# Performance work log

Measured on AMD Instinct MI355X. Metric: run time of the kernel, lower is better.

## Reference

```python
import jax, jax.numpy as jnp
import numpy as np

B, C, H, W = 4, 256, 128, 128
HEADS, KD, VD = 8, 64, 64
EPS = 1e-5


def setup_inputs() -> dict:
    key = jax.random.key(0)
    ks = jax.random.split(key, 5)
    s = 0.02
    return {
        "x": jax.random.normal(ks[0], (B, C, H, W), dtype=jnp.float32),
        "wq": jax.random.normal(ks[1], (HEADS * KD, C), dtype=jnp.float32) * s,
        "bq": jnp.zeros((HEADS * KD,), dtype=jnp.float32),
        "wk": jax.random.normal(ks[2], (HEADS * KD, C), dtype=jnp.float32) * s,
        "bk": jnp.zeros((HEADS * KD,), dtype=jnp.float32),
        "wv": jax.random.normal(ks[3], (HEADS * VD, C), dtype=jnp.float32) * s,
        "bv": jnp.zeros((HEADS * VD,), dtype=jnp.float32),
        "wo": jax.random.normal(ks[4], (C, HEADS * VD), dtype=jnp.float32) * s,
        "bo": jnp.zeros((C,), dtype=jnp.float32),
        "g_q": jnp.ones((KD,), dtype=jnp.float32),
        "be_q": jnp.zeros((KD,), dtype=jnp.float32),
        "g_k": jnp.ones((KD,), dtype=jnp.float32),
        "be_k": jnp.zeros((KD,), dtype=jnp.float32),
        "g_v": jnp.ones((VD,), dtype=jnp.float32),
        "be_v": jnp.zeros((VD,), dtype=jnp.float32),
    }


def _conv1x1(t, w, b):
    # t: [B,C,H,W], w: [O,C] -> [B,O,H,W]
    return jnp.einsum("bchw,oc->bohw", t, w) + b[None, :, None, None]


def _ln_dim(t, g, be):
    # LayerNorm over the per-head feature axis (axis=2) of [B,heads,dim,N]
    mu = jnp.mean(t, axis=2, keepdims=True)
    var = jnp.var(t, axis=2, keepdims=True)
    return (t - mu) * jax.lax.rsqrt(var + EPS) * g[None, None, :, None] + be[None, None, :, None]


def reference(x, wq, bq, wk, bk, wv, bv, wo, bo, g_q, be_q, g_k, be_k, g_v, be_v):
    b, c, h, w = x.shape
    n = h * w
    # context defaults to x
    q = _conv1x1(x, wq, bq).reshape(b, HEADS, KD, n)
    k = _conv1x1(x, wk, bk).reshape(b, HEADS, KD, n)
    v = _conv1x1(x, wv, bv).reshape(b, HEADS, VD, n)
    q = _ln_dim(q, g_q, be_q)
    k = _ln_dim(k, g_k, be_k)
    v = _ln_dim(v, g_v, be_v)
    q = jax.nn.softmax(q * (KD ** -0.25), axis=2)  # softmax over key_dim
    k = jax.nn.softmax(k, axis=3)                  # softmax over N
    ctx = jnp.einsum("bhkn,bhvn->bhkv", k, v)      # [B,heads,KD,VD]
    out = jnp.einsum("bhkn,bhkv->bhvn", q, ctx)    # [B,heads,VD,N]
    out = out.reshape(b, HEADS * VD, h, w)
    return _conv1x1(out, wo, bo)
```

## Files before the change

### kernel.cpp

```cpp
#include <hip/hip_runtime.h>
#include <hip/hip_bf16.h>
#include <stdint.h>

typedef unsigned short u16;
typedef __attribute__((__vector_size__(16))) short s16x8;
typedef __attribute__((__vector_size__(16))) float f32x4;

#define N_ 16384
#define C_ 256

__device__ __forceinline__ float bf2f(u16 u) {
    union { uint32_t i; float f; } v; v.i = ((uint32_t)u) << 16; return v.f;
}
__device__ __forceinline__ u16 f2bf(float f) {
    union { uint32_t i; float f; } v; v.f = f;
    uint32_t u = v.i;
    return (u16)((u + 0x7FFFu + ((u >> 16) & 1u)) >> 16);
}

__device__ __forceinline__ void gl_lds16(const u16* g, u16* l) {
    __builtin_amdgcn_global_load_lds((__attribute__((address_space(1))) void*)g,
                                     (__attribute__((address_space(3))) void*)l,
                                     16, 0, 0);
}

__global__ __launch_bounds__(256) void zero_kernel(float* __restrict__ p, int n) {
    int i = blockIdx.x * 256 + threadIdx.x;
    if (i < n) p[i] = 0.f;
}

__global__ __launch_bounds__(256) void transpose_kernel(const float* __restrict__ x,
                                                        u16* __restrict__ xT) {
    __shared__ float T[64][65];
    int tid = threadIdx.x;
    int n0 = blockIdx.x * 64, c0 = blockIdx.y * 64, b = blockIdx.z;
    const float* xp = x + (size_t)b * C_ * N_;
    for (int it = 0; it < 16; it++) {
        int idx = it * 256 + tid;
        int c = idx >> 6, n = idx & 63;
        T[c][n] = xp[(size_t)(c0 + c) * N_ + n0 + n];
    }
    __syncthreads();
    u16* op = xT + (size_t)b * N_ * C_;
    for (int it = 0; it < 8; it++) {
        int idx = it * 256 + tid;
        int n = idx >> 5, c2 = (idx & 31) * 2;
        uint32_t lo = f2bf(T[c2][n]);
        uint32_t hi = f2bf(T[c2 + 1][n]);
        *(uint32_t*)&op[(size_t)(n0 + n) * C_ + c0 + c2] = lo | (hi << 16);
    }
}

__global__ __launch_bounds__(256) void cvtw_kernel(const float* __restrict__ wq,
                                                   const float* __restrict__ wk,
                                                   const float* __restrict__ wv,
                                                   u16* __restrict__ wb) {
    int m = blockIdx.y;
    const float* s = m == 0 ? wq : (m == 1 ? wk : wv);
    int i = blockIdx.x * 256 + threadIdx.x;
    wb[(size_t)m * 131072 + i] = f2bf(s[i]);
}


#define STAGE2(WSRC, XSRC, LDW, KC, CUR) {                                         \
    int koff_ = (KC) * 64 + sc8;                                                   \
    _Pragma("unroll")                                                              \
    for (int i_ = 0; i_ < 4; i_++) {                                               \
        int row_ = (wid * 4 + i_) * 8 + srow;                                      \
        gl_lds16(&(WSRC)[(size_t)row_ * (LDW) + koff_], &SH[CUR][(wid * 4 + i_) * 512]);      \
        gl_lds16(&(XSRC)[(size_t)row_ * (LDW) + koff_], &SH[2 + (CUR)][(wid * 4 + i_) * 512]); \
    } }

__global__ __launch_bounds__(256) void kvctx_kernel(
    const u16* __restrict__ xT, const u16* __restrict__ wb,
    const float* __restrict__ bk, const float* __restrict__ bv,
    const float* __restrict__ gk, const float* __restrict__ bek,
    const float* __restrict__ gv, const float* __restrict__ bev,
    float* __restrict__ ctxp, float* __restrict__ rs)
{
    __shared__ u16 SH[4][8704];
    int tid = threadIdx.x;
    int lane = tid & 63, wid = tid >> 6;
    int quad = lane >> 4, l15 = lane & 15;
    int wm = wid >> 1, wn = wid & 1;
    int ns = blockIdx.x, h = blockIdx.y, b = blockIdx.z;

    const u16* wsrcw = wb + (size_t)(1 + (wid >> 1)) * 131072
                          + ((size_t)h * 64 + (size_t)(wid & 1) * 32) * 256;

    int srow = lane >> 3;
    int sc8  = ((lane & 7) ^ srow) * 8;

#define STAGEF(XP, KC, CUR) {                                                      \
    int koff_ = (KC) * 64 + sc8;                                                   \
    _Pragma("unroll")                                                              \
    for (int i_ = 0; i_ < 4; i_++) {                                               \
        int ri_ = i_ * 8 + srow;                                                   \
        gl_lds16(&wsrcw[(size_t)ri_ * 256 + koff_], &SH[CUR][(wid * 4 + i_) * 512]); \
        gl_lds16(&(XP)[(size_t)(wid * 32 + ri_) * 256 + koff_], &SH[2 + (CUR)][(wid * 4 + i_) * 512]); \
    } }

    const float* bptr  = wm ? bv  : bk;
    const float* gptr  = wm ? gv  : gk;
    const float* beptr = wm ? bev : bek;
    float bB_[4], gB[4], eB[4];
#pragma unroll
    for (int nf = 0; nf < 4; nf++) {
        int rl = nf * 16 + l15;
        bB_[nf] = bptr[h * 64 + rl];
        gB[nf]  = gptr[rl];
        eB[nf]  = beptr[rl];
    }

    f32x4 cacc[4][4];
#pragma unroll
    for (int i = 0; i < 4; i++)
#pragma unroll
        for (int j = 0; j < 4; j++) cacc[i][j] = (f32x4){0.f, 0.f, 0.f, 0.f};
    float rs_acc[4] = {0.f, 0.f, 0.f, 0.f};

    {
        const u16* x0 = xT + ((size_t)b * N_ + (size_t)(ns * 8) * 128) * 256;
        STAGEF(x0, 0, 0);
    }
    __syncthreads();

    for (int t = 0; t < 8; t++) {
        const u16* xcur = xT + ((size_t)b * N_ + (size_t)(ns * 8 + t) * 128) * 256;

        f32x4 acc[4][4];
#pragma unroll
        for (int i = 0; i < 4; i++)
#pragma unroll
            for (int j = 0; j < 4; j++) acc[i][j] = (f32x4){0.f, 0.f, 0.f, 0.f};

        for (int kc = 0; kc < 4; kc++) {
            int cur = (kc + t) & 1;
            if (kc < 3) STAGEF(xcur, kc + 1, cur ^ 1);
            const u16* Wb = &SH[cur][0];
            const u16* Xb = &SH[2 + cur][0];
#pragma unroll
            for (int ks = 0; ks < 2; ks++) {
                int cc = ks * 4 + quad;
                s16x8 af[4], bf[4];
#pragma unroll
                for (int f = 0; f < 4; f++) {
                    int ar = wn * 64 + f * 16 + l15;
                    int br = wm * 64 + f * 16 + l15;
                    af[f] = *(const s16x8*)&Xb[ar * 64 + ((cc ^ (ar & 7)) * 8)];
                    bf[f] = *(const s16x8*)&Wb[br * 64 + ((cc ^ (br & 7)) * 8)];
                }
#pragma unroll
                for (int i = 0; i < 4; i++)
#pragma unroll
                    for (int j = 0; j < 4; j++)
                        acc[i][j] = __builtin_amdgcn_mfma_f32_16x16x32_bf16(af[i], bf[j], acc[i][j], 0, 0, 0);
            }
            if (kc < 3) __syncthreads();
        }

#pragma unroll
        for (int mf = 0; mf < 4; mf++)
#pragma unroll
            for (int nf = 0; nf < 4; nf++)
#pragma unroll
                for (int r = 0; r < 4; r++) acc[mf][nf][r] += bB_[nf];
        float sa[4][4], sb[4][4];
#pragma unroll
        for (int mf = 0; mf < 4; mf++)
#pragma unroll
            for (int r = 0; r < 4; r++) {
                float s = 0.f, s2 = 0.f;
#pragma unroll
                for (int nf = 0; nf < 4; nf++) { float v = acc[mf][nf][r]; s += v; s2 += v * v; }
                sa[mf][r] = s; sb[mf][r] = s2;
            }
#pragma unroll
        for (int msk = 1; msk <= 8; msk <<= 1)
#pragma unroll
            for (int mf = 0; mf < 4; mf++)
#pragma unroll
                for (int r = 0; r < 4; r++) {
                    sa[mf][r] += __shfl_xor(sa[mf][r], msk);
                    sb[mf][r] += __shfl_xor(sb[mf][r], msk);
                }
#pragma unroll
        for (int mf = 0; mf < 4; mf++)
#pragma unroll
            for (int r = 0; r < 4; r++) {
                float mu = sa[mf][r] * (1.f / 64.f);
                float rstd = rsqrtf(sb[mf][r] * (1.f / 64.f) - mu * mu + 1e-5f);
#pragma unroll
                for (int nf = 0; nf < 4; nf++)
                    acc[mf][nf][r] = (acc[mf][nf][r] - mu) * rstd * gB[nf] + eB[nf];
            }
        if (wm == 0) {
#pragma unroll
            for (int mf = 0; mf < 4; mf++)
#pragma unroll
                for (int nf = 0; nf < 4; nf++)
#pragma unroll
                    for (int r = 0; r < 4; r++) acc[mf][nf][r] = __expf(acc[mf][nf][r]);
#pragma unroll
            for (int nf = 0; nf < 4; nf++) {
                float s = 0.f;
#pragma unroll
                for (int mf = 0; mf < 4; mf++)
#pragma unroll
                    for (int r = 0; r < 4; r++) s += acc[mf][nf][r];
                s += __shfl_xor(s, 16); s += __shfl_xor(s, 32);
                rs_acc[nf] += s;
            }
        }

        int esb = t & 1;
        u16* ES = &SH[esb][0];
        u16* VS = &SH[2 + esb][0];
        {
            u16* st = wm ? VS : ES;
#pragma unroll
            for (int mf = 0; mf < 4; mf++)
#pragma unroll
                for (int nf = 0; nf < 4; nf++) {
                    int rh = nf * 16 + l15;
                    int ln = wn * 64 + mf * 16 + quad * 4;
                    int c  = ln >> 3;
                    int off = rh * 128 + ((c ^ (rh & 15)) * 8) + (ln & 7);
                    uint64_t w0 = (uint64_t)f2bf(acc[mf][nf][0]) | ((uint64_t)f2bf(acc[mf][nf][1]) << 16) |
                                  ((uint64_t)f2bf(acc[mf][nf][2]) << 32) | ((uint64_t)f2bf(acc[mf][nf][3]) << 48);
                    *(uint64_t*)&st[off] = w0;
                }
        }
        __syncthreads();

        if (t < 7) {
            const u16* xnext = xT + ((size_t)b * N_ + (size_t)(ns * 8 + t + 1) * 128) * 256;
            STAGEF(xnext, 0, (t + 1) & 1);
        }
        {
            int cc = wid * 4 + quad;
            s16x8 caf[4], cbf[4];
#pragma unroll
            for (int f = 0; f < 4; f++) {
                int off = (f * 16 + l15) * 128 + ((cc ^ l15) * 8);
                caf[f] = *(const s16x8*)&ES[off];
                cbf[f] = *(const s16x8*)&VS[off];
            }
#pragma unroll
            for (int i = 0; i < 4; i++)
#pragma unroll
                for (int j = 0; j < 4; j++)
                    cacc[i][j] = __builtin_amdgcn_mfma_f32_16x16x32_bf16(caf[i], cbf[j], cacc[i][j], 0, 0, 0);
        }
        __syncthreads();
    }

    if (wm == 0 && quad == 0) {
#pragma unroll
        for (int nf = 0; nf < 4; nf++)
            atomicAdd(&rs[(size_t)b * 512 + h * 64 + nf * 16 + l15], rs_acc[nf]);
    }
    {
        float* CTXW = (float*)((char*)SH + (size_t)wid * 17408);
#pragma unroll
        for (int mf = 0; mf < 4; mf++)
#pragma unroll
            for (int nf = 0; nf < 4; nf++) {
                int kd = mf * 16 + quad * 4, vd = nf * 16 + l15;
                *(f32x4*)&CTXW[vd * 68 + kd] = cacc[mf][nf];
            }
    }
    __syncthreads();
    {
        int vd = tid >> 2, kd0 = (tid & 3) * 16;
        const float* C0 = (const float*)((char*)SH);
        const float* C1 = (const float*)((char*)SH + 17408);
        const float* C2 = (const float*)((char*)SH + 34816);
        const float* C3 = (const float*)((char*)SH + 52224);
        float* gp = ctxp + (((size_t)(b * 8 + h) * 16 + ns) * 4096) + vd * 64 + kd0;
#pragma unroll
        for (int j4 = 0; j4 < 4; j4++) {
            int o = vd * 68 + kd0 + j4 * 4;
            f32x4 s = *(const f32x4*)&C0[o];
            s += *(const f32x4*)&C1[o];
            s += *(const f32x4*)&C2[o];
            s += *(const f32x4*)&C3[o];
            *(f32x4*)&gp[j4 * 4] = s;
        }
    }
#undef STAGEF
}

__global__ __launch_bounds__(256) void q_kernel(
    const u16* __restrict__ xT, const u16* __restrict__ wb,
    const float* __restrict__ bq, const float* __restrict__ gq, const float* __restrict__ beq,
    u16* __restrict__ qT)
{
    __shared__ u16 SH[4][8192];
    int tid = threadIdx.x;
    int lane = tid & 63, wid = tid >> 6;
    int quad = lane >> 4, l15 = lane & 15;
    int wm = wid >> 1, wn = wid & 1;
    int bx = blockIdx.x, pair = blockIdx.y, b = blockIdx.z;
    int r0 = pair * 128;
    int n0 = bx * 128;

    const u16* wsrc = wb + (size_t)r0 * 256;
    const u16* xsrc = xT + ((size_t)b * N_ + n0) * 256;

    f32x4 acc[4][4];
#pragma unroll
    for (int i = 0; i < 4; i++)
#pragma unroll
        for (int j = 0; j < 4; j++) acc[i][j] = (f32x4){0.f, 0.f, 0.f, 0.f};

    int srow = lane >> 3;
    int sc8  = ((lane & 7) ^ srow) * 8;

    STAGE2(wsrc, xsrc, 256, 0, 0);
    __syncthreads();
    for (int kc = 0; kc < 4; kc++) {
        int cur = kc & 1;
        if (kc < 3) STAGE2(wsrc, xsrc, 256, kc + 1, cur ^ 1);
        const u16* Wb = &SH[cur][0];
        const u16* Xb = &SH[2 + cur][0];
#pragma unroll
        for (int ks = 0; ks < 2; ks++) {
            int cc = ks * 4 + quad;
            s16x8 af[4], bf[4];
#pragma unroll
            for (int f = 0; f < 4; f++) {
                int ar = wm * 64 + f * 16 + l15;
                int br = wn * 64 + f * 16 + l15;
                af[f] = *(const s16x8*)&Wb[ar * 64 + ((cc ^ (ar & 7)) * 8)];
                bf[f] = *(const s16x8*)&Xb[br * 64 + ((cc ^ (br & 7)) * 8)];
            }
#pragma unroll
            for (int i = 0; i < 4; i++)
#pragma unroll
                for (int j = 0; j < 4; j++)
                    acc[i][j] = __builtin_amdgcn_mfma_f32_16x16x32_bf16(af[i], bf[j], acc[i][j], 0, 0, 0);
        }
        if (kc < 3) __syncthreads();
    }

    float bA[4][4], gA[4][4], eA[4][4];
#pragma unroll
    for (int mf = 0; mf < 4; mf++)
#pragma unroll
        for (int r = 0; r < 4; r++) {
            int rl = mf * 16 + quad * 4 + r;
            bA[mf][r] = bq[r0 + wm * 64 + rl];
            gA[mf][r] = gq[rl];
            eA[mf][r] = beq[rl];
        }
#pragma unroll
    for (int mf = 0; mf < 4; mf++)
#pragma unroll
        for (int nf = 0; nf < 4; nf++)
#pragma unroll
            for (int r = 0; r < 4; r++) acc[mf][nf][r] += bA[mf][r];
#pragma unroll
    for (int nf = 0; nf < 4; nf++) {
        float s = 0.f, s2 = 0.f;
#pragma unroll
        for (int mf = 0; mf < 4; mf++)
#pragma unroll
            for (int r = 0; r < 4; r++) { float v = acc[mf][nf][r]; s += v; s2 += v * v; }
        s  += __shfl_xor(s, 16);  s  += __shfl_xor(s, 32);
        s2 += __shfl_xor(s2, 16); s2 += __shfl_xor(s2, 32);
        float mu = s * (1.f / 64.f);
        float rstd = rsqrtf(s2 * (1.f / 64.f) - mu * mu + 1e-5f);
#pragma unroll
        for (int mf = 0; mf < 4; mf++)
#pragma unroll
            for (int r = 0; r < 4; r++)
                acc[mf][nf][r] = (acc[mf][nf][r] - mu) * rstd * gA[mf][r] + eA[mf][r];
    }
    const float s_q = 0.35355339059327373f;
#pragma unroll
    for (int nf = 0; nf < 4; nf++) {
        float m = -1e30f;
#pragma unroll
        for (int mf = 0; mf < 4; mf++)
#pragma unroll
            for (int r = 0; r < 4; r++) { acc[mf][nf][r] *= s_q; m = fmaxf(m, acc[mf][nf][r]); }
        m = fmaxf(m, __shfl_xor(m, 16)); m = fmaxf(m, __shfl_xor(m, 32));
        float d = 0.f;
#pragma unroll
        for (int mf = 0; mf < 4; mf++)
#pragma unroll
            for (int r = 0; r < 4; r++) { float e = __expf(acc[mf][nf][r] - m); acc[mf][nf][r] = e; d += e; }
        d += __shfl_xor(d, 16); d += __shfl_xor(d, 32);
        float inv = 1.f / d;
#pragma unroll
        for (int mf = 0; mf < 4; mf++)
#pragma unroll
            for (int r = 0; r < 4; r++) acc[mf][nf][r] *= inv;
    }
    u16* st = (wn == 0) ? &SH[0][0] : &SH[2][0];
#pragma unroll
    for (int mf = 0; mf < 4; mf++)
#pragma unroll
        for (int nf = 0; nf < 4; nf++) {
            int nl = nf * 16 + l15;
            int gl = wm * 64 + mf * 16 + quad * 4;
            int c  = gl >> 3;
            int off = nl * 128 + ((c ^ (nl & 15)) * 8) + (gl & 7);
            uint64_t w0 = (uint64_t)f2bf(acc[mf][nf][0]) | ((uint64_t)f2bf(acc[mf][nf][1]) << 16) |
                          ((uint64_t)f2bf(acc[mf][nf][2]) << 32) | ((uint64_t)f2bf(acc[mf][nf][3]) << 48);
            *(uint64_t*)&st[off] = w0;
        }
    __syncthreads();
    {
        u16* qp = qT + (size_t)b * N_ * 512;
#pragma unroll
        for (int i = 0; i < 8; i++) {
            int idx = i * 256 + tid;
            int n = idx >> 4, cp = idx & 15;
            const u16* src = (n < 64) ? &SH[0][0] : &SH[2][0];
            int nl = n & 63;
            s16x8 v = *(const s16x8*)&src[nl * 128 + ((cp ^ (nl & 15)) * 8)];
            *(s16x8*)&qp[(size_t)(n0 + n) * 512 + r0 + cp * 8] = v;
        }
    }
}

__global__ __launch_bounds__(256) void weff_kernel(
    const float* __restrict__ ctxp, const float* __restrict__ rs,
    const float* __restrict__ wo, u16* __restrict__ Weffb)
{
    __shared__ float CT[16][65];
    int tid = threadIdx.x;
    int h = blockIdx.x, b = blockIdx.y, kc = blockIdx.z;
    for (int i = tid; i < 1024; i += 256) {
        int kdl = i >> 6, vd = i & 63;
        int kd = kc * 16 + kdl;
        float s = 0.f;
#pragma unroll
        for (int sl = 0; sl < 16; sl++)
            s += ctxp[(((size_t)(b * 8 + h) * 16 + sl) * 4096) + vd * 64 + kd];
        CT[kdl][vd] = s / rs[(size_t)b * 512 + h * 64 + kd];
    }
    __syncthreads();
    int c = tid;
    float wrow[64];
    const float4* wp = (const float4*)(wo + (size_t)c * 512 + h * 64);
#pragma unroll
    for (int i = 0; i < 16; i++) { float4 t = wp[i]; wrow[i*4] = t.x; wrow[i*4+1] = t.y; wrow[i*4+2] = t.z; wrow[i*4+3] = t.w; }
    for (int kdl = 0; kdl < 16; kdl++) {
        float s = 0.f;
#pragma unroll
        for (int vd = 0; vd < 64; vd++) s += wrow[vd] * CT[kdl][vd];
        Weffb[((size_t)b * 256 + c) * 512 + h * 64 + kc * 16 + kdl] = f2bf(s);
    }
}

__global__ __launch_bounds__(256) void out_kernel(
    const u16* __restrict__ Weffb, const u16* __restrict__ qT,
    const float* __restrict__ bo, float* __restrict__ out)
{
    __shared__ u16 SH[4][8192];
    int tid = threadIdx.x;
    int lane = tid & 63, wid = tid >> 6;
    int quad = lane >> 4, l15 = lane & 15;
    int wm = wid >> 1, wn = wid & 1;
    int n0 = blockIdx.x * 128, c0 = blockIdx.y * 128, b = blockIdx.z;
    const u16* asrc = Weffb + ((size_t)b * 256 + c0) * 512;
    const u16* bsrc = qT + ((size_t)b * N_ + n0) * 512;

    f32x4 acc[4][4];
#pragma unroll
    for (int i = 0; i < 4; i++)
#pragma unroll
        for (int j = 0; j < 4; j++) acc[i][j] = (f32x4){0.f, 0.f, 0.f, 0.f};

    int srow = lane >> 3;
    int sc8  = ((lane & 7) ^ srow) * 8;

    STAGE2(asrc, bsrc, 512, 0, 0);
    __syncthreads();
    for (int kc = 0; kc < 8; kc++) {
        int cur = kc & 1;
        if (kc < 7) STAGE2(asrc, bsrc, 512, kc + 1, cur ^ 1);
        const u16* Wb = &SH[cur][0];
        const u16* Xb = &SH[2 + cur][0];
#pragma unroll
        for (int ks = 0; ks < 2; ks++) {
            int cc = ks * 4 + quad;
            s16x8 af[4], bf[4];
#pragma unroll
            for (int f = 0; f < 4; f++) {
                int ar = wm * 64 + f * 16 + l15;
                int br = wn * 64 + f * 16 + l15;
                af[f] = *(const s16x8*)&Wb[ar * 64 + ((cc ^ (ar & 7)) * 8)];
                bf[f] = *(const s16x8*)&Xb[br * 64 + ((cc ^ (br & 7)) * 8)];
            }
#pragma unroll
            for (int i = 0; i < 4; i++)
#pragma unroll
                for (int j = 0; j < 4; j++)
                    acc[i][j] = __builtin_amdgcn_mfma_f32_16x16x32_bf16(af[i], bf[j], acc[i][j], 0, 0, 0);
        }
        if (kc < 7) __syncthreads();
    }
#pragma unroll
    for (int mf = 0; mf < 4; mf++)
#pragma unroll
        for (int r = 0; r < 4; r++) {
            int c = c0 + wm * 64 + mf * 16 + quad * 4 + r;
            float bov = bo[c];
#pragma unroll
            for (int nf = 0; nf < 4; nf++)
                out[((size_t)b * 256 + c) * N_ + n0 + wn * 64 + nf * 16 + l15] = acc[mf][nf][r] + bov;
        }
}

extern "C" void kernel_launch(void* const* d_in, const int* in_sizes, int n_in,
                              void* d_out, int out_size, void* d_ws, size_t ws_size,
                              hipStream_t stream) {
    const float* x   = (const float*)d_in[0];
    const float* wq  = (const float*)d_in[1];
    const float* bq  = (const float*)d_in[2];
    const float* wk  = (const float*)d_in[3];
    const float* bk  = (const float*)d_in[4];
    const float* wv  = (const float*)d_in[5];
    const float* bv  = (const float*)d_in[6];
    const float* wo  = (const float*)d_in[7];
    const float* bo  = (const float*)d_in[8];
    const float* gq  = (const float*)d_in[9];
    const float* beq = (const float*)d_in[10];
    const float* gk  = (const float*)d_in[11];
    const float* bek = (const float*)d_in[12];
    const float* gv  = (const float*)d_in[13];
    const float* bev = (const float*)d_in[14];
    float* out = (float*)d_out;

    char* ws = (char*)d_ws;
    u16* xT      = (u16*)(ws);
    u16* wb      = (u16*)(ws + 33554432ULL);
    u16* qT      = (u16*)(ws + 34340864ULL);
    float* ctxp  = (float*)(ws + 101449728ULL);
    float* rs    = (float*)(ws + 169082880ULL);
    u16* Weffb   = (u16*)(ws + 169091072ULL);

    cvtw_kernel<<<dim3(512, 3), 256, 0, stream>>>(wq, wk, wv, wb);
    transpose_kernel<<<dim3(256, 4, 4), 256, 0, stream>>>(x, xT);
    zero_kernel<<<dim3(8), 256, 0, stream>>>(rs, 2048);

    kvctx_kernel<<<dim3(16, 8, 4), 256, 0, stream>>>(
        xT, wb, bk, bv, gk, bek, gv, bev, ctxp, rs);

    q_kernel<<<dim3(128, 4, 4), 256, 0, stream>>>(xT, wb, bq, gq, beq, qT);

    weff_kernel<<<dim3(8, 4, 4), 256, 0, stream>>>(ctxp, rs, wo, Weffb);

    out_kernel<<<dim3(128, 2, 4), 256, 0, stream>>>(Weffb, qT, bo, out);
}
```

Before: 342.2 us.

## Split kvctx over more N-slices and widen out_kernel tiles to full channel dim

kvctx_kernel now processes 4 tiles per block instead of 8 and launches twice as many blocks, writing 32 partial context slices that weff_kernel sums. out_kernel computes all 256 output channels per block (8x4 MFMA tiles per wave), loading each qT tile once instead of twice, but drops the double-buffered staging in favour of single-buffer load-then-sync. The aim is more parallelism in the context reduction and less redundant qT traffic, at the cost of more partial-sum memory, higher register pressure and lost load/compute overlap in out_kernel.

```diff
diff --git a/kernel.cpp b/kernel.cpp
--- a/kernel.cpp
+++ b/kernel.cpp
@@ -120,13 +120,13 @@
     float rs_acc[4] = {0.f, 0.f, 0.f, 0.f};
 
     {
-        const u16* x0 = xT + ((size_t)b * N_ + (size_t)(ns * 8) * 128) * 256;
+        const u16* x0 = xT + ((size_t)b * N_ + (size_t)(ns * 4) * 128) * 256;
         STAGEF(x0, 0, 0);
     }
     __syncthreads();
 
-    for (int t = 0; t < 8; t++) {
-        const u16* xcur = xT + ((size_t)b * N_ + (size_t)(ns * 8 + t) * 128) * 256;
+    for (int t = 0; t < 4; t++) {
+        const u16* xcur = xT + ((size_t)b * N_ + (size_t)(ns * 4 + t) * 128) * 256;
 
         f32x4 acc[4][4];
 #pragma unroll
@@ -233,8 +233,8 @@
         }
         __syncthreads();
 
-        if (t < 7) {
-            const u16* xnext = xT + ((size_t)b * N_ + (size_t)(ns * 8 + t + 1) * 128) * 256;
+        if (t < 3) {
+            const u16* xnext = xT + ((size_t)b * N_ + (size_t)(ns * 4 + t + 1) * 128) * 256;
             STAGEF(xnext, 0, (t + 1) & 1);
         }
         {
@@ -277,7 +277,7 @@
         const float* C1 = (const float*)((char*)SH + 17408);
         const float* C2 = (const float*)((char*)SH + 34816);
         const float* C3 = (const float*)((char*)SH + 52224);
-        float* gp = ctxp + (((size_t)(b * 8 + h) * 16 + ns) * 4096) + vd * 64 + kd0;
+        float* gp = ctxp + (((size_t)(b * 8 + h) * 32 + ns) * 4096) + vd * 64 + kd0;
 #pragma unroll
         for (int j4 = 0; j4 < 4; j4++) {
             int o = vd * 68 + kd0 + j4 * 4;
@@ -438,8 +438,8 @@
         int kd = kc * 16 + kdl;
         float s = 0.f;
 #pragma unroll
-        for (int sl = 0; sl < 16; sl++)
-            s += ctxp[(((size_t)(b * 8 + h) * 16 + sl) * 4096) + vd * 64 + kd];
+        for (int sl = 0; sl < 32; sl++)
+            s += ctxp[(((size_t)(b * 8 + h) * 32 + sl) * 4096) + vd * 64 + kd];
         CT[kdl][vd] = s / rs[(size_t)b * 512 + h * 64 + kd];
     }
     __syncthreads();
@@ -460,44 +460,54 @@
     const u16* __restrict__ Weffb, const u16* __restrict__ qT,
     const float* __restrict__ bo, float* __restrict__ out)
 {
-    __shared__ u16 SH[4][8192];
+    __shared__ u16 WS[256 * 64];
+    __shared__ u16 XS[128 * 64];
     int tid = threadIdx.x;
     int lane = tid & 63, wid = tid >> 6;
     int quad = lane >> 4, l15 = lane & 15;
     int wm = wid >> 1, wn = wid & 1;
-    int n0 = blockIdx.x * 128, c0 = blockIdx.y * 128, b = blockIdx.z;
-    const u16* asrc = Weffb + ((size_t)b * 256 + c0) * 512;
+    int n0 = blockIdx.x * 128, b = blockIdx.y;
+    const u16* asrc = Weffb + (size_t)b * 256 * 512;
     const u16* bsrc = qT + ((size_t)b * N_ + n0) * 512;
 
-    f32x4 acc[4][4];
-#pragma unroll
-    for (int i = 0; i < 4; i++)
+    f32x4 acc[8][4];
+#pragma unroll
+    for (int i = 0; i < 8; i++)
 #pragma unroll
         for (int j = 0; j < 4; j++) acc[i][j] = (f32x4){0.f, 0.f, 0.f, 0.f};
 
     int srow = lane >> 3;
     int sc8  = ((lane & 7) ^ srow) * 8;
 
-    STAGE2(asrc, bsrc, 512, 0, 0);
-    __syncthreads();
     for (int kc = 0; kc < 8; kc++) {
-        int cur = kc & 1;
-        if (kc < 7) STAGE2(asrc, bsrc, 512, kc + 1, cur ^ 1);
-        const u16* Wb = &SH[cur][0];
-        const u16* Xb = &SH[2 + cur][0];
+        int koff = kc * 64 + sc8;
+#pragma unroll
+        for (int i = 0; i < 8; i++) {
+            int row = wid * 64 + i * 8 + srow;
+            gl_lds16(&asrc[(size_t)row * 512 + koff], &WS[(wid * 8 + i) * 512]);
+        }
+#pragma unroll
+        for (int i = 0; i < 4; i++) {
+            int row = wid * 32 + i * 8 + srow;
+            gl_lds16(&bsrc[(size_t)row * 512 + koff], &XS[(wid * 4 + i) * 512]);
+        }
+        __syncthreads();
 #pragma unroll
         for (int ks = 0; ks < 2; ks++) {
             int cc = ks * 4 + quad;
-            s16x8 af[4], bf[4];
+            s16x8 af[8], bf[4];
+#pragma unroll
+            for (int f = 0; f < 8; f++) {
+                int ar = wm * 128 + f * 16 + l15;
+                af[f] = *(const s16x8*)&WS[ar * 64 + ((cc ^ (ar & 7)) * 8)];
+            }
 #pragma unroll
             for (int f = 0; f < 4; f++) {
-                int ar = wm * 64 + f * 16 + l15;
                 int br = wn * 64 + f * 16 + l15;
-                af[f] = *(const s16x8*)&Wb[ar * 64 + ((cc ^ (ar & 7)) * 8)];
-                bf[f] = *(const s16x8*)&Xb[br * 64 + ((cc ^ (br & 7)) * 8)];
-            }
-#pragma unroll
-            for (int i = 0; i < 4; i++)
+                bf[f] = *(const s16x8*)&XS[br * 64 + ((cc ^ (br & 7)) * 8)];
+            }
+#pragma unroll
+            for (int i = 0; i < 8; i++)
 #pragma unroll
                 for (int j = 0; j < 4; j++)
                     acc[i][j] = __builtin_amdgcn_mfma_f32_16x16x32_bf16(af[i], bf[j], acc[i][j], 0, 0, 0);
@@ -505,10 +515,10 @@
         if (kc < 7) __syncthreads();
     }
 #pragma unroll
-    for (int mf = 0; mf < 4; mf++)
+    for (int mf = 0; mf < 8; mf++)
 #pragma unroll
         for (int r = 0; r < 4; r++) {
-            int c = c0 + wm * 64 + mf * 16 + quad * 4 + r;
+            int c = wm * 128 + mf * 16 + quad * 4 + r;
             float bov = bo[c];
 #pragma unroll
             for (int nf = 0; nf < 4; nf++)
@@ -548,12 +558,12 @@
     transpose_kernel<<<dim3(256, 4, 4), 256, 0, stream>>>(x, xT);
     zero_kernel<<<dim3(8), 256, 0, stream>>>(rs, 2048);
 
-    kvctx_kernel<<<dim3(16, 8, 4), 256, 0, stream>>>(
+    kvctx_kernel<<<dim3(32, 8, 4), 256, 0, stream>>>(
         xT, wb, bk, bv, gk, bek, gv, bev, ctxp, rs);
 
     q_kernel<<<dim3(128, 4, 4), 256, 0, stream>>>(xT, wb, bq, gq, beq, qT);
 
     weff_kernel<<<dim3(8, 4, 4), 256, 0, stream>>>(ctxp, rs, wo, Weffb);
 
-    out_kernel<<<dim3(128, 2, 4), 256, 0, stream>>>(Weffb, qT, bo, out);
-}
+    out_kernel<<<dim3(128, 4), 256, 0, stream>>>(Weffb, qT, bo, out);
+}
```

Measured after the change: 369.3 us. +7.9%, slower.

## Triple-buffer activation tiles with explicit vmcnt waits in q and out GEMMs

Applied to the files above, without the earlier changes.

Replaces the double-buffered LDS staging in q_kernel and out_kernel with separate weight (2-slot) and activation (3-slot) buffers. Activation loads are issued two k-steps ahead, and hand-written s_barrier plus s_waitcnt vmcnt counts replace __syncthreads so that outstanding global-to-LDS loads can overlap the MFMA work. This is meant to hide global memory latency in the streamed operand, at the cost of more LDS (80KB vs 64KB per block), possibly lower occupancy, and fragile vmcnt bookkeeping.

```diff
diff --git a/kernel.cpp b/kernel.cpp
--- a/kernel.cpp
+++ b/kernel.cpp
@@ -61,15 +61,6 @@
     wb[(size_t)m * 131072 + i] = f2bf(s[i]);
 }
 
-
-#define STAGE2(WSRC, XSRC, LDW, KC, CUR) {                                         \
-    int koff_ = (KC) * 64 + sc8;                                                   \
-    _Pragma("unroll")                                                              \
-    for (int i_ = 0; i_ < 4; i_++) {                                               \
-        int row_ = (wid * 4 + i_) * 8 + srow;                                      \
-        gl_lds16(&(WSRC)[(size_t)row_ * (LDW) + koff_], &SH[CUR][(wid * 4 + i_) * 512]);      \
-        gl_lds16(&(XSRC)[(size_t)row_ * (LDW) + koff_], &SH[2 + (CUR)][(wid * 4 + i_) * 512]); \
-    } }
 
 __global__ __launch_bounds__(256) void kvctx_kernel(
     const u16* __restrict__ xT, const u16* __restrict__ wb,
@@ -291,12 +282,29 @@
 #undef STAGEF
 }
 
+
+#define SW3(SRC, LDW, KC, SLOT) {                                                  \
+    int koff_ = (KC) * 64 + sc8;                                                   \
+    _Pragma("unroll")                                                              \
+    for (int i_ = 0; i_ < 4; i_++) {                                               \
+        int row_ = (wid * 4 + i_) * 8 + srow;                                      \
+        gl_lds16(&(SRC)[(size_t)row_ * (LDW) + koff_], &WS3[SLOT][(wid * 4 + i_) * 512]); \
+    } }
+#define SX3(SRC, LDW, KC, SLOT) {                                                  \
+    int koff_ = (KC) * 64 + sc8;                                                   \
+    _Pragma("unroll")                                                              \
+    for (int i_ = 0; i_ < 4; i_++) {                                               \
+        int row_ = (wid * 4 + i_) * 8 + srow;                                      \
+        gl_lds16(&(SRC)[(size_t)row_ * (LDW) + koff_], &XS3[SLOT][(wid * 4 + i_) * 512]); \
+    } }
+
 __global__ __launch_bounds__(256) void q_kernel(
     const u16* __restrict__ xT, const u16* __restrict__ wb,
     const float* __restrict__ bq, const float* __restrict__ gq, const float* __restrict__ beq,
     u16* __restrict__ qT)
 {
-    __shared__ u16 SH[4][8192];
+    __shared__ u16 WS3[2][8192];
+    __shared__ u16 XS3[3][8192];
     int tid = threadIdx.x;
     int lane = tid & 63, wid = tid >> 6;
     int quad = lane >> 4, l15 = lane & 15;
@@ -317,13 +325,21 @@
     int srow = lane >> 3;
     int sc8  = ((lane & 7) ^ srow) * 8;
 
-    STAGE2(wsrc, xsrc, 256, 0, 0);
-    __syncthreads();
+    SX3(xsrc, 256, 0, 0);
+    SW3(wsrc, 256, 0, 0);
+    SX3(xsrc, 256, 1, 1);
+#pragma unroll
     for (int kc = 0; kc < 4; kc++) {
-        int cur = kc & 1;
-        if (kc < 3) STAGE2(wsrc, xsrc, 256, kc + 1, cur ^ 1);
-        const u16* Wb = &SH[cur][0];
-        const u16* Xb = &SH[2 + cur][0];
+        asm volatile("s_barrier" ::: "memory");
+        if (kc + 1 < 4) SW3(wsrc, 256, kc + 1, (kc + 1) & 1);
+        if (kc + 2 < 4) SX3(xsrc, 256, kc + 2, (kc + 2) % 3);
+        if (kc + 2 < 4)      { asm volatile("s_waitcnt vmcnt(12)" ::: "memory"); }
+        else if (kc + 1 < 4) { asm volatile("s_waitcnt vmcnt(8)"  ::: "memory"); }
+        else                 { asm volatile("s_waitcnt vmcnt(0)"  ::: "memory"); }
+        asm volatile("s_barrier" ::: "memory");
+        __builtin_amdgcn_sched_barrier(0);
+        const u16* Wb = &WS3[kc & 1][0];
+        const u16* Xb = &XS3[kc % 3][0];
 #pragma unroll
         for (int ks = 0; ks < 2; ks++) {
             int cc = ks * 4 + quad;
@@ -341,7 +357,6 @@
                 for (int j = 0; j < 4; j++)
                     acc[i][j] = __builtin_amdgcn_mfma_f32_16x16x32_bf16(af[i], bf[j], acc[i][j], 0, 0, 0);
         }
-        if (kc < 3) __syncthreads();
     }
 
     float bA[4][4], gA[4][4], eA[4][4];
@@ -398,7 +413,8 @@
 #pragma unroll
             for (int r = 0; r < 4; r++) acc[mf][nf][r] *= inv;
     }
-    u16* st = (wn == 0) ? &SH[0][0] : &SH[2][0];
+    __syncthreads();
+    u16* st = (wn == 0) ? &XS3[0][0] : &XS3[1][0];
 #pragma unroll
     for (int mf = 0; mf < 4; mf++)
 #pragma unroll
@@ -418,7 +434,7 @@
         for (int i = 0; i < 8; i++) {
             int idx = i * 256 + tid;
             int n = idx >> 4, cp = idx & 15;
-            const u16* src = (n < 64) ? &SH[0][0] : &SH[2][0];
+            const u16* src = (n < 64) ? &XS3[0][0] : &XS3[1][0];
             int nl = n & 63;
             s16x8 v = *(const s16x8*)&src[nl * 128 + ((cp ^ (nl & 15)) * 8)];
             *(s16x8*)&qp[(size_t)(n0 + n) * 512 + r0 + cp * 8] = v;
@@ -460,7 +476,8 @@
     const u16* __restrict__ Weffb, const u16* __restrict__ qT,
     const float* __restrict__ bo, float* __restrict__ out)
 {
-    __shared__ u16 SH[4][8192];
+    __shared__ u16 WS3[2][8192];
+    __shared__ u16 XS3[3][8192];
     int tid = threadIdx.x;
     int lane = tid & 63, wid = tid >> 6;
     int quad = lane >> 4, l15 = lane & 15;
@@ -478,13 +495,21 @@
     int srow = lane >> 3;
     int sc8  = ((lane & 7) ^ srow) * 8;
 
-    STAGE2(asrc, bsrc, 512, 0, 0);
-    __syncthreads();
+    SX3(bsrc, 512, 0, 0);
+    SW3(asrc, 512, 0, 0);
+    SX3(bsrc, 512, 1, 1);
+#pragma unroll
     for (int kc = 0; kc < 8; kc++) {
-        int cur = kc & 1;
-        if (kc < 7) STAGE2(asrc, bsrc, 512, kc + 1, cur ^ 1);
-        const u16* Wb = &SH[cur][0];
-        const u16* Xb = &SH[2 + cur][0];
+        asm volatile("s_barrier" ::: "memory");
+        if (kc + 1 < 8) SW3(asrc, 512, kc + 1, (kc + 1) & 1);
+        if (kc + 2 < 8) SX3(bsrc, 512, kc + 2, (kc + 2) % 3);
+        if (kc + 2 < 8)      { asm volatile("s_waitcnt vmcnt(12)" ::: "memory"); }
+        else if (kc + 1 < 8) { asm volatile("s_waitcnt vmcnt(8)"  ::: "memory"); }
+        else                 { asm volatile("s_waitcnt vmcnt(0)"  ::: "memory"); }
+        asm volatile("s_barrier" ::: "memory");
+        __builtin_amdgcn_sched_barrier(0);
+        const u16* Wb = &WS3[kc & 1][0];
+        const u16* Xb = &XS3[kc % 3][0];
 #pragma unroll
         for (int ks = 0; ks < 2; ks++) {
             int cc = ks * 4 + quad;
@@ -502,7 +527,6 @@
                 for (int j = 0; j < 4; j++)
                     acc[i][j] = __builtin_amdgcn_mfma_f32_16x16x32_bf16(af[i], bf[j], acc[i][j], 0, 0, 0);
         }
-        if (kc < 7) __syncthreads();
     }
 #pragma unroll
     for (int mf = 0; mf < 4; mf++)
```

Result: no change. 344.3 us (+0.6%).

## Fuse Q projection with output GEMM to avoid qT round-trip; fold zeroing into cvtw

Applied to the files above, without the earlier changes.

Merges the Q projection, LayerNorm and softmax kernel with the output projection GEMM, so each block computes Q for a 128-column tile and consumes it straight from LDS against Weff. This removes the global write and re-read of the bf16 qT tensor and one launch. The zero kernel for rs is also folded into the weight-conversion kernel. In exchange the grid shrinks from 1024 to 512 blocks, each block's output tile grows to all 256 channels with 32 accumulator vectors per thread (more register pressure), and Weff is reloaded without double buffering.

```diff
diff --git a/kernel.cpp b/kernel.cpp
--- a/kernel.cpp
+++ b/kernel.cpp
@@ -22,11 +22,6 @@
     __builtin_amdgcn_global_load_lds((__attribute__((address_space(1))) void*)g,
                                      (__attribute__((address_space(3))) void*)l,
                                      16, 0, 0);
-}
-
-__global__ __launch_bounds__(256) void zero_kernel(float* __restrict__ p, int n) {
-    int i = blockIdx.x * 256 + threadIdx.x;
-    if (i < n) p[i] = 0.f;
 }
 
 __global__ __launch_bounds__(256) void transpose_kernel(const float* __restrict__ x,
@@ -54,22 +49,15 @@
 __global__ __launch_bounds__(256) void cvtw_kernel(const float* __restrict__ wq,
                                                    const float* __restrict__ wk,
                                                    const float* __restrict__ wv,
-                                                   u16* __restrict__ wb) {
+                                                   u16* __restrict__ wb,
+                                                   float* __restrict__ rs) {
     int m = blockIdx.y;
+    if (m == 0 && blockIdx.x < 8) rs[blockIdx.x * 256 + threadIdx.x] = 0.f;
     const float* s = m == 0 ? wq : (m == 1 ? wk : wv);
     int i = blockIdx.x * 256 + threadIdx.x;
     wb[(size_t)m * 131072 + i] = f2bf(s[i]);
 }
 
-
-#define STAGE2(WSRC, XSRC, LDW, KC, CUR) {                                         \
-    int koff_ = (KC) * 64 + sc8;                                                   \
-    _Pragma("unroll")                                                              \
-    for (int i_ = 0; i_ < 4; i_++) {                                               \
-        int row_ = (wid * 4 + i_) * 8 + srow;                                      \
-        gl_lds16(&(WSRC)[(size_t)row_ * (LDW) + koff_], &SH[CUR][(wid * 4 + i_) * 512]);      \
-        gl_lds16(&(XSRC)[(size_t)row_ * (LDW) + koff_], &SH[2 + (CUR)][(wid * 4 + i_) * 512]); \
-    } }
 
 __global__ __launch_bounds__(256) void kvctx_kernel(
     const u16* __restrict__ xT, const u16* __restrict__ wb,
@@ -291,141 +279,6 @@
 #undef STAGEF
 }
 
-__global__ __launch_bounds__(256) void q_kernel(
-    const u16* __restrict__ xT, const u16* __restrict__ wb,
-    const float* __restrict__ bq, const float* __restrict__ gq, const float* __restrict__ beq,
-    u16* __restrict__ qT)
-{
-    __shared__ u16 SH[4][8192];
-    int tid = threadIdx.x;
-    int lane = tid & 63, wid = tid >> 6;
-    int quad = lane >> 4, l15 = lane & 15;
-    int wm = wid >> 1, wn = wid & 1;
-    int bx = blockIdx.x, pair = blockIdx.y, b = blockIdx.z;
-    int r0 = pair * 128;
-    int n0 = bx * 128;
-
-    const u16* wsrc = wb + (size_t)r0 * 256;
-    const u16* xsrc = xT + ((size_t)b * N_ + n0) * 256;
-
-    f32x4 acc[4][4];
-#pragma unroll
-    for (int i = 0; i < 4; i++)
-#pragma unroll
-        for (int j = 0; j < 4; j++) acc[i][j] = (f32x4){0.f, 0.f, 0.f, 0.f};
-
-    int srow = lane >> 3;
-    int sc8  = ((lane & 7) ^ srow) * 8;
-
-    STAGE2(wsrc, xsrc, 256, 0, 0);
-    __syncthreads();
-    for (int kc = 0; kc < 4; kc++) {
-        int cur = kc & 1;
-        if (kc < 3) STAGE2(wsrc, xsrc, 256, kc + 1, cur ^ 1);
-        const u16* Wb = &SH[cur][0];
-        const u16* Xb = &SH[2 + cur][0];
-#pragma unroll
-        for (int ks = 0; ks < 2; ks++) {
-            int cc = ks * 4 + quad;
-            s16x8 af[4], bf[4];
-#pragma unroll
-            for (int f = 0; f < 4; f++) {
-                int ar = wm * 64 + f * 16 + l15;
-                int br = wn * 64 + f * 16 + l15;
-                af[f] = *(const s16x8*)&Wb[ar * 64 + ((cc ^ (ar & 7)) * 8)];
-                bf[f] = *(const s16x8*)&Xb[br * 64 + ((cc ^ (br & 7)) * 8)];
-            }
-#pragma unroll
-            for (int i = 0; i < 4; i++)
-#pragma unroll
-                for (int j = 0; j < 4; j++)
-                    acc[i][j] = __builtin_amdgcn_mfma_f32_16x16x32_bf16(af[i], bf[j], acc[i][j], 0, 0, 0);
-        }
-        if (kc < 3) __syncthreads();
-    }
-
-    float bA[4][4], gA[4][4], eA[4][4];
-#pragma unroll
-    for (int mf = 0; mf < 4; mf++)
-#pragma unroll
-        for (int r = 0; r < 4; r++) {
-            int rl = mf * 16 + quad * 4 + r;
-            bA[mf][r] = bq[r0 + wm * 64 + rl];
-            gA[mf][r] = gq[rl];
-            eA[mf][r] = beq[rl];
-        }
-#pragma unroll
-    for (int mf = 0; mf < 4; mf++)
-#pragma unroll
-        for (int nf = 0; nf < 4; nf++)
-#pragma unroll
-            for (int r = 0; r < 4; r++) acc[mf][nf][r] += bA[mf][r];
-#pragma unroll
-    for (int nf = 0; nf < 4; nf++) {
-        float s = 0.f, s2 = 0.f;
-#pragma unroll
-        for (int mf = 0; mf < 4; mf++)
-#pragma unroll
-            for (int r = 0; r < 4; r++) { float v = acc[mf][nf][r]; s += v; s2 += v * v; }
-        s  += __shfl_xor(s, 16);  s  += __shfl_xor(s, 32);
-        s2 += __shfl_xor(s2, 16); s2 += __shfl_xor(s2, 32);
-        float mu = s * (1.f / 64.f);
-        float rstd = rsqrtf(s2 * (1.f / 64.f) - mu * mu + 1e-5f);
-#pragma unroll
-        for (int mf = 0; mf < 4; mf++)
-#pragma unroll
-            for (int r = 0; r < 4; r++)
-                acc[mf][nf][r] = (acc[mf][nf][r] - mu) * rstd * gA[mf][r] + eA[mf][r];
-    }
-    const float s_q = 0.35355339059327373f;
-#pragma unroll
-    for (int nf = 0; nf < 4; nf++) {
-        float m = -1e30f;
-#pragma unroll
-        for (int mf = 0; mf < 4; mf++)
-#pragma unroll
-            for (int r = 0; r < 4; r++) { acc[mf][nf][r] *= s_q; m = fmaxf(m, acc[mf][nf][r]); }
-        m = fmaxf(m, __shfl_xor(m, 16)); m = fmaxf(m, __shfl_xor(m, 32));
-        float d = 0.f;
-#pragma unroll
-        for (int mf = 0; mf < 4; mf++)
-#pragma unroll
-            for (int r = 0; r < 4; r++) { float e = __expf(acc[mf][nf][r] - m); acc[mf][nf][r] = e; d += e; }
-        d += __shfl_xor(d, 16); d += __shfl_xor(d, 32);
-        float inv = 1.f / d;
-#pragma unroll
-        for (int mf = 0; mf < 4; mf++)
-#pragma unroll
-            for (int r = 0; r < 4; r++) acc[mf][nf][r] *= inv;
-    }
-    u16* st = (wn == 0) ? &SH[0][0] : &SH[2][0];
-#pragma unroll
-    for (int mf = 0; mf < 4; mf++)
-#pragma unroll
-        for (int nf = 0; nf < 4; nf++) {
-            int nl = nf * 16 + l15;
-            int gl = wm * 64 + mf * 16 + quad * 4;
-            int c  = gl >> 3;
-            int off = nl * 128 + ((c ^ (nl & 15)) * 8) + (gl & 7);
-            uint64_t w0 = (uint64_t)f2bf(acc[mf][nf][0]) | ((uint64_t)f2bf(acc[mf][nf][1]) << 16) |
-                          ((uint64_t)f2bf(acc[mf][nf][2]) << 32) | ((uint64_t)f2bf(acc[mf][nf][3]) << 48);
-            *(uint64_t*)&st[off] = w0;
-        }
-    __syncthreads();
-    {
-        u16* qp = qT + (size_t)b * N_ * 512;
-#pragma unroll
-        for (int i = 0; i < 8; i++) {
-            int idx = i * 256 + tid;
-            int n = idx >> 4, cp = idx & 15;
-            const u16* src = (n < 64) ? &SH[0][0] : &SH[2][0];
-            int nl = n & 63;
-            s16x8 v = *(const s16x8*)&src[nl * 128 + ((cp ^ (nl & 15)) * 8)];
-            *(s16x8*)&qp[(size_t)(n0 + n) * 512 + r0 + cp * 8] = v;
-        }
-    }
-}
-
 __global__ __launch_bounds__(256) void weff_kernel(
     const float* __restrict__ ctxp, const float* __restrict__ rs,
     const float* __restrict__ wo, u16* __restrict__ Weffb)
@@ -456,63 +309,191 @@
     }
 }
 
-__global__ __launch_bounds__(256) void out_kernel(
-    const u16* __restrict__ Weffb, const u16* __restrict__ qT,
-    const float* __restrict__ bo, float* __restrict__ out)
+__global__ __launch_bounds__(256) void qout_kernel(
+    const u16* __restrict__ xT, const u16* __restrict__ wb,
+    const float* __restrict__ bq, const float* __restrict__ gq, const float* __restrict__ beq,
+    const u16* __restrict__ Weffb, const float* __restrict__ bo, float* __restrict__ out)
 {
-    __shared__ u16 SH[4][8192];
+    __shared__ u16 WS[2][8192];
+    __shared__ u16 QB[2][8192];
     int tid = threadIdx.x;
     int lane = tid & 63, wid = tid >> 6;
     int quad = lane >> 4, l15 = lane & 15;
     int wm = wid >> 1, wn = wid & 1;
-    int n0 = blockIdx.x * 128, c0 = blockIdx.y * 128, b = blockIdx.z;
-    const u16* asrc = Weffb + ((size_t)b * 256 + c0) * 512;
-    const u16* bsrc = qT + ((size_t)b * N_ + n0) * 512;
-
-    f32x4 acc[4][4];
-#pragma unroll
-    for (int i = 0; i < 4; i++)
-#pragma unroll
-        for (int j = 0; j < 4; j++) acc[i][j] = (f32x4){0.f, 0.f, 0.f, 0.f};
-
+    int nt = blockIdx.x, b = blockIdx.y;
+    int n0 = nt * 128;
+
+    const u16* xsrc = xT + ((size_t)b * N_ + n0) * 256;
     int srow = lane >> 3;
     int sc8  = ((lane & 7) ^ srow) * 8;
 
-    STAGE2(asrc, bsrc, 512, 0, 0);
-    __syncthreads();
-    for (int kc = 0; kc < 8; kc++) {
-        int cur = kc & 1;
-        if (kc < 7) STAGE2(asrc, bsrc, 512, kc + 1, cur ^ 1);
-        const u16* Wb = &SH[cur][0];
-        const u16* Xb = &SH[2 + cur][0];
-#pragma unroll
-        for (int ks = 0; ks < 2; ks++) {
-            int cc = ks * 4 + quad;
-            s16x8 af[4], bf[4];
-#pragma unroll
-            for (int f = 0; f < 4; f++) {
-                int ar = wm * 64 + f * 16 + l15;
-                int br = wn * 64 + f * 16 + l15;
-                af[f] = *(const s16x8*)&Wb[ar * 64 + ((cc ^ (ar & 7)) * 8)];
-                bf[f] = *(const s16x8*)&Xb[br * 64 + ((cc ^ (br & 7)) * 8)];
-            }
-#pragma unroll
-            for (int i = 0; i < 4; i++)
-#pragma unroll
-                for (int j = 0; j < 4; j++)
-                    acc[i][j] = __builtin_amdgcn_mfma_f32_16x16x32_bf16(af[i], bf[j], acc[i][j], 0, 0, 0);
-        }
-        if (kc < 7) __syncthreads();
-    }
-#pragma unroll
-    for (int mf = 0; mf < 4; mf++)
+    f32x4 oacc[8][4];
+#pragma unroll
+    for (int i = 0; i < 8; i++)
+#pragma unroll
+        for (int j = 0; j < 4; j++) oacc[i][j] = (f32x4){0.f, 0.f, 0.f, 0.f};
+
+#define QSTAGE(WSRC, KC, CUR) {                                                    \
+    int koff_ = (KC) * 64 + sc8;                                                   \
+    _Pragma("unroll")                                                              \
+    for (int i_ = 0; i_ < 4; i_++) {                                               \
+        int row_ = (wid * 4 + i_) * 8 + srow;                                      \
+        gl_lds16(&(WSRC)[(size_t)row_ * 256 + koff_], &WS[CUR][(wid * 4 + i_) * 512]);  \
+        gl_lds16(&xsrc[(size_t)row_ * 256 + koff_], &QB[CUR][(wid * 4 + i_) * 512]);    \
+    } }
+
+    for (int p = 0; p < 4; p++) {
+        const u16* wsrc = wb + (size_t)(p * 128) * 256;
+        f32x4 qacc[4][4];
+#pragma unroll
+        for (int i = 0; i < 4; i++)
+#pragma unroll
+            for (int j = 0; j < 4; j++) qacc[i][j] = (f32x4){0.f, 0.f, 0.f, 0.f};
+
+        QSTAGE(wsrc, 0, 0);
+        __syncthreads();
+        for (int kc = 0; kc < 4; kc++) {
+            int cur = kc & 1;
+            if (kc < 3) QSTAGE(wsrc, kc + 1, cur ^ 1);
+            const u16* Wb = &WS[cur][0];
+            const u16* Xb = &QB[cur][0];
+#pragma unroll
+            for (int ks = 0; ks < 2; ks++) {
+                int cc = ks * 4 + quad;
+                s16x8 af[4], bf[4];
+#pragma unroll
+                for (int f = 0; f < 4; f++) {
+                    int ar = wm * 64 + f * 16 + l15;
+                    int br = wn * 64 + f * 16 + l15;
+                    af[f] = *(const s16x8*)&Wb[ar * 64 + ((cc ^ (ar & 7)) * 8)];
+                    bf[f] = *(const s16x8*)&Xb[br * 64 + ((cc ^ (br & 7)) * 8)];
+                }
+#pragma unroll
+                for (int i = 0; i < 4; i++)
+#pragma unroll
+                    for (int j = 0; j < 4; j++)
+                        qacc[i][j] = __builtin_amdgcn_mfma_f32_16x16x32_bf16(af[i], bf[j], qacc[i][j], 0, 0, 0);
+            }
+            if (kc < 3) __syncthreads();
+        }
+
+        int r0 = p * 128;
+        float bA[4][4], gA[4][4], eA[4][4];
+#pragma unroll
+        for (int mf = 0; mf < 4; mf++)
+#pragma unroll
+            for (int r = 0; r < 4; r++) {
+                int rl = mf * 16 + quad * 4 + r;
+                bA[mf][r] = bq[r0 + wm * 64 + rl];
+                gA[mf][r] = gq[rl];
+                eA[mf][r] = beq[rl];
+            }
+#pragma unroll
+        for (int mf = 0; mf < 4; mf++)
+#pragma unroll
+            for (int nf = 0; nf < 4; nf++)
+#pragma unroll
+                for (int r = 0; r < 4; r++) qacc[mf][nf][r] += bA[mf][r];
+#pragma unroll
+        for (int nf = 0; nf < 4; nf++) {
+            float s = 0.f, s2 = 0.f;
+#pragma unroll
+            for (int mf = 0; mf < 4; mf++)
+#pragma unroll
+                for (int r = 0; r < 4; r++) { float v = qacc[mf][nf][r]; s += v; s2 += v * v; }
+            s  += __shfl_xor(s, 16);  s  += __shfl_xor(s, 32);
+            s2 += __shfl_xor(s2, 16); s2 += __shfl_xor(s2, 32);
+            float mu = s * (1.f / 64.f);
+            float rstd = rsqrtf(s2 * (1.f / 64.f) - mu * mu + 1e-5f);
+#pragma unroll
+            for (int mf = 0; mf < 4; mf++)
+#pragma unroll
+                for (int r = 0; r < 4; r++)
+                    qacc[mf][nf][r] = (qacc[mf][nf][r] - mu) * rstd * gA[mf][r] + eA[mf][r];
+        }
+        const float s_q = 0.35355339059327373f;
+#pragma unroll
+        for (int nf = 0; nf < 4; nf++) {
+            float m = -1e30f;
+#pragma unroll
+            for (int mf = 0; mf < 4; mf++)
+#pragma unroll
+                for (int r = 0; r < 4; r++) { qacc[mf][nf][r] *= s_q; m = fmaxf(m, qacc[mf][nf][r]); }
+            m = fmaxf(m, __shfl_xor(m, 16)); m = fmaxf(m, __shfl_xor(m, 32));
+            float d = 0.f;
+#pragma unroll
+            for (int mf = 0; mf < 4; mf++)
+#pragma unroll
+                for (int r = 0; r < 4; r++) { float e = __expf(qacc[mf][nf][r] - m); qacc[mf][nf][r] = e; d += e; }
+            d += __shfl_xor(d, 16); d += __shfl_xor(d, 32);
+            float inv = 1.f / d;
+#pragma unroll
+            for (int mf = 0; mf < 4; mf++)
+#pragma unroll
+                for (int r = 0; r < 4; r++) qacc[mf][nf][r] *= inv;
+        }
+        __syncthreads();
+        {
+            u16* st = &QB[wn][0];
+#pragma unroll
+            for (int mf = 0; mf < 4; mf++)
+#pragma unroll
+                for (int nf = 0; nf < 4; nf++) {
+                    int nl = nf * 16 + l15;
+                    int gl = wm * 64 + mf * 16 + quad * 4;
+                    int c  = gl >> 3;
+                    int off = nl * 128 + ((c ^ (nl & 15)) * 8) + (gl & 7);
+                    uint64_t w0 = (uint64_t)f2bf(qacc[mf][nf][0]) | ((uint64_t)f2bf(qacc[mf][nf][1]) << 16) |
+                                  ((uint64_t)f2bf(qacc[mf][nf][2]) << 32) | ((uint64_t)f2bf(qacc[mf][nf][3]) << 48);
+                    *(uint64_t*)&st[off] = w0;
+                }
+        }
+        __syncthreads();
+
+#pragma unroll
+        for (int sub = 0; sub < 2; sub++) {
+#pragma unroll
+            for (int i_ = 0; i_ < 8; i_++) {
+                int row = wid * 64 + i_ * 8 + srow;
+                gl_lds16(&Weffb[((size_t)b * 256 + row) * 512 + p * 128 + sub * 64 + sc8],
+                         &WS[wid >> 1][((wid & 1) * 64 + i_ * 8) * 64]);
+            }
+            __syncthreads();
+#pragma unroll
+            for (int ks = 0; ks < 2; ks++) {
+                int cca = ks * 4 + quad;
+                int ccb = sub * 8 + ks * 4 + quad;
+                s16x8 af[8], bf[4];
+#pragma unroll
+                for (int f = 0; f < 8; f++) {
+                    int ar = f * 16 + l15;
+                    af[f] = *(const s16x8*)&WS[wm][ar * 64 + ((cca ^ (ar & 7)) * 8)];
+                }
+#pragma unroll
+                for (int f = 0; f < 4; f++) {
+                    int br = f * 16 + l15;
+                    bf[f] = *(const s16x8*)&QB[wn][br * 128 + ((ccb ^ (br & 15)) * 8)];
+                }
+#pragma unroll
+                for (int i = 0; i < 8; i++)
+#pragma unroll
+                    for (int j = 0; j < 4; j++)
+                        oacc[i][j] = __builtin_amdgcn_mfma_f32_16x16x32_bf16(af[i], bf[j], oacc[i][j], 0, 0, 0);
+            }
+            __syncthreads();
+        }
+    }
+#undef QSTAGE
+
+#pragma unroll
+    for (int mf = 0; mf < 8; mf++)
 #pragma unroll
         for (int r = 0; r < 4; r++) {
-            int c = c0 + wm * 64 + mf * 16 + quad * 4 + r;
+            int c = wm * 128 + mf * 16 + quad * 4 + r;
             float bov = bo[c];
 #pragma unroll
             for (int nf = 0; nf < 4; nf++)
-                out[((size_t)b * 256 + c) * N_ + n0 + wn * 64 + nf * 16 + l15] = acc[mf][nf][r] + bov;
+                out[((size_t)b * 256 + c) * N_ + n0 + wn * 64 + nf * 16 + l15] = oacc[mf][nf][r] + bov;
         }
 }
 
@@ -539,21 +520,17 @@
     char* ws = (char*)d_ws;
     u16* xT      = (u16*)(ws);
     u16* wb      = (u16*)(ws + 33554432ULL);
-    u16* qT      = (u16*)(ws + 34340864ULL);
     float* ctxp  = (float*)(ws + 101449728ULL);
     float* rs    = (float*)(ws + 169082880ULL);
     u16* Weffb   = (u16*)(ws + 169091072ULL);
 
-    cvtw_kernel<<<dim3(512, 3), 256, 0, stream>>>(wq, wk, wv, wb);
+    cvtw_kernel<<<dim3(512, 3), 256, 0, stream>>>(wq, wk, wv, wb, rs);
     transpose_kernel<<<dim3(256, 4, 4), 256, 0, stream>>>(x, xT);
-    zero_kernel<<<dim3(8), 256, 0, stream>>>(rs, 2048);
 
     kvctx_kernel<<<dim3(16, 8, 4), 256, 0, stream>>>(
         xT, wb, bk, bv, gk, bek, gv, bev, ctxp, rs);
 
-    q_kernel<<<dim3(128, 4, 4), 256, 0, stream>>>(xT, wb, bq, gq, beq, qT);
-
     weff_kernel<<<dim3(8, 4, 4), 256, 0, stream>>>(ctxp, rs, wo, Weffb);
 
-    out_kernel<<<dim3(128, 2, 4), 256, 0, stream>>>(Weffb, qT, bo, out);
-}
+    qout_kernel<<<dim3(128, 4), 256, 0, stream>>>(xT, wb, bq, gq, beq, Weffb, bo, out);
+}
```

After: 346.4 us. About the same (+1.2%).
